# Kernel optimization log

Hardware: AMD Instinct MI355X
Metric: run time of the kernel (lower is better)

Reference implementation:

```python
import jax, jax.numpy as jnp
import numpy as np

N, D_IN, D_H, D_OUT, M = 256, 768, 768, 512, 100000


def setup_inputs() -> dict:
    key = jax.random.key(0)
    ks = jax.random.split(key, 8)
    img_feats = jax.random.normal(ks[0], (N, D_IN), dtype=jnp.float32)
    w1 = jax.random.normal(ks[1], (D_H, D_IN), dtype=jnp.float32) * (1.0 / np.sqrt(D_IN))
    b1 = jax.random.normal(ks[2], (D_H,), dtype=jnp.float32) * 0.01
    w2 = jax.random.normal(ks[3], (D_OUT, D_H), dtype=jnp.float32) * (1.0 / np.sqrt(D_H))
    b2 = jax.random.normal(ks[4], (D_OUT,), dtype=jnp.float32) * 0.01
    logit_scale = jnp.asarray(np.log(1.0 / 0.07), dtype=jnp.float32)
    loc = jax.random.normal(ks[5], (M, D_OUT), dtype=jnp.float32)
    loc_feats = loc / jnp.linalg.norm(loc, axis=1, keepdims=True)  # pre-normalized gallery
    gps_gallery = jax.random.uniform(ks[6], (M, 2), dtype=jnp.float32, minval=-90.0, maxval=90.0)
    return {
        "img_feats": img_feats, "w1": w1, "b1": b1, "w2": w2, "b2": b2,
        "logit_scale": logit_scale, "loc_feats": loc_feats,
        "gps_gallery": gps_gallery, "top_k": 5,
    }


def reference(img_feats, w1, b1, w2, b2, logit_scale, loc_feats, gps_gallery, top_k):
    # Tsfm MLP head: Linear -> ReLU -> Linear
    h = jax.nn.relu(img_feats @ w1.T + b1)            # [N, D_H]
    img = h @ w2.T + b2                               # [N, D_OUT]
    # F.normalize(dim=1)
    img_n = img / jnp.linalg.norm(img, axis=1, keepdims=True)
    # forward_cached: scaled cosine-similarity logits against 100K gallery
    logits = jnp.exp(logit_scale) * (img_n @ loc_feats.T)  # [N, M]
    # predict: softmax over full gallery row, then top-k retrieval
    probs = jax.nn.softmax(logits, axis=-1)
    top_vals, top_idx = jax.lax.top_k(probs, top_k)   # [N, k]
    top_pred_gps = gps_gallery[top_idx[0]]            # [k, 2] (first image, as in original)
    top_pred_prob = top_vals[0]                       # [k]
    return (logits, top_pred_gps, top_pred_prob)
```

## Files before the change

kernel.cpp:

```cpp
#include <hip/hip_runtime.h>
#include <math.h>

#define N_IMG 256
#define DIN   768
#define DH    768
#define DOUT  512
#define M_GAL 100000
#define CAP   2048
#define MT    784

typedef __bf16 bf16_t;
typedef __bf16 bf16x8 __attribute__((ext_vector_type(8)));
typedef float  f32x4  __attribute__((ext_vector_type(4)));

#define OFF_H      0
#define OFF_IMG    (N_IMG*DH)
#define OFF_IMGN   (OFF_IMG  + N_IMG*DOUT)
#define OFF_IMGT   (OFF_IMGN + N_IMG*DOUT)
#define OFF_STATS  (OFF_IMGT + N_IMG*DOUT/2)
#define OFF_CIDX   (OFF_STATS + 4)
#define OFF_CVAL   (OFF_CIDX + CAP)

#define OUT_GPS  ((size_t)N_IMG * (size_t)M_GAL)
#define OUT_PROB (OUT_GPS + 10)

__device__ inline unsigned fkey(float x) {
  unsigned u = __float_as_uint(x);
  return (u & 0x80000000u) ? ~u : (u | 0x80000000u);
}
__device__ inline float fkey_inv(unsigned k) {
  unsigned u = (k & 0x80000000u) ? (k ^ 0x80000000u) : ~k;
  return __uint_as_float(u);
}

template<int KDIM, int NCOLS, bool RELU>
__global__ __launch_bounds__(256) void mlp_gemm(const float* __restrict__ A,
    const float* __restrict__ B, const float* __restrict__ bias,
    float* __restrict__ C, unsigned* stats_init) {
  if (stats_init && blockIdx.x == 0 && blockIdx.y == 0 && threadIdx.x == 0) {
    stats_init[0] = 0u; stats_init[1] = 0u; stats_init[2] = 0u;
  }
  __shared__ float As[32][34];
  __shared__ float Bs[32][34];
  const int t  = threadIdx.x;
  const int rowbase = blockIdx.y * 32;
  const int colbase = blockIdx.x * 32;
  const int sm = t >> 3;
  const int kc = (t & 7) << 2;
  const int ty = t >> 4, tx = t & 15;
  float a00 = 0.f, a01 = 0.f, a10 = 0.f, a11 = 0.f;
  for (int kt = 0; kt < KDIM; kt += 32) {
    float4 av = *(const float4*)(A + (size_t)(rowbase + sm) * KDIM + kt + kc);
    float4 bv = *(const float4*)(B + (size_t)(colbase + sm) * KDIM + kt + kc);
    __syncthreads();
    As[kc+0][sm] = av.x; As[kc+1][sm] = av.y; As[kc+2][sm] = av.z; As[kc+3][sm] = av.w;
    Bs[kc+0][sm] = bv.x; Bs[kc+1][sm] = bv.y; Bs[kc+2][sm] = bv.z; Bs[kc+3][sm] = bv.w;
    __syncthreads();
#pragma unroll
    for (int j = 0; j < 32; ++j) {
      float2 a = *(const float2*)(&As[j][2*ty]);
      float2 b = *(const float2*)(&Bs[j][2*tx]);
      a00 = fmaf(a.x, b.x, a00); a01 = fmaf(a.x, b.y, a01);
      a10 = fmaf(a.y, b.x, a10); a11 = fmaf(a.y, b.y, a11);
    }
  }
  const int r0 = rowbase + 2*ty;
  const int c0 = colbase + 2*tx;
  const float bb0 = bias[c0], bb1 = bias[c0+1];
  float v00 = a00 + bb0, v01 = a01 + bb1, v10 = a10 + bb0, v11 = a11 + bb1;
  if (RELU) {
    v00 = fmaxf(v00, 0.f); v01 = fmaxf(v01, 0.f);
    v10 = fmaxf(v10, 0.f); v11 = fmaxf(v11, 0.f);
  }
  C[(size_t)r0*NCOLS + c0]       = v00; C[(size_t)r0*NCOLS + c0 + 1]     = v01;
  C[(size_t)(r0+1)*NCOLS + c0]   = v10; C[(size_t)(r0+1)*NCOLS + c0 + 1] = v11;
}

__global__ __launch_bounds__(256) void norm_cast_kernel(const float* __restrict__ img,
    float* __restrict__ img_n, bf16_t* __restrict__ img_t) {
  const int row = blockIdx.x, t = threadIdx.x;
  const float v0 = img[row*DOUT + t];
  const float v1 = img[row*DOUT + 256 + t];
  float s = v0*v0 + v1*v1;
  for (int o = 32; o > 0; o >>= 1) s += __shfl_down(s, o);
  __shared__ float ws4[4];
  if ((t & 63) == 0) ws4[t >> 6] = s;
  __syncthreads();
  const float tot = ws4[0] + ws4[1] + ws4[2] + ws4[3];
  const float inv = 1.0f / sqrtf(tot);
  const float n0 = v0 * inv, n1 = v1 * inv;
  img_n[row*DOUT + t]       = n0;
  img_n[row*DOUT + 256 + t] = n1;
  const int k0 = t, k1 = t + 256;
  img_t[(((k0 >> 3)*N_IMG) + row)*8 + (k0 & 7)] = (bf16_t)n0;
  img_t[(((k1 >> 3)*N_IMG) + row)*8 + (k1 & 7)] = (bf16_t)n1;
}

__global__ __launch_bounds__(256, 4) void logits_kernel(const float* __restrict__ loc,
    const bf16_t* __restrict__ img_t, const float* __restrict__ ls,
    float* __restrict__ out, float* __restrict__ sumexp, unsigned* __restrict__ maxkey) {
  __shared__ bf16_t Asl[32 * 64 * 8];
  const int t = threadIdx.x;
  const int w = t >> 6, l = t & 63;
  const int bx = blockIdx.x;
  const int mtile = (bx & 7) + (bx >> 5) * 8;
  const int ntile = (bx >> 3) & 3;
  const int mb = mtile * 128;
  const int nb = ntile * 64;
  const int lr = l & 15, lq = l >> 4;
  const int mw = mb + w * 32;

  const float* bp[2];
#pragma unroll
  for (int j = 0; j < 2; ++j) {
    int m = mw + j * 16 + lr;
    m = m < M_GAL ? m : (M_GAL - 1);
    bp[j] = loc + (size_t)m * 512 + lq * 8;
  }

  f32x4 acc[4][2];
#pragma unroll
  for (int i = 0; i < 4; ++i)
#pragma unroll
    for (int j = 0; j < 2; ++j)
      acc[i][j] = (f32x4){0.f, 0.f, 0.f, 0.f};

  float4 B0[3][2], B1[3][2];

#define ISSUE(kt) {                                                  \
    const int s_ = (kt) % 3;                                         \
    _Pragma("unroll")                                                \
    for (int j_ = 0; j_ < 2; ++j_) {                                 \
      const float* p_ = bp[j_] + (kt) * 32;                          \
      B0[s_][j_] = *(const float4*)p_;                               \
      B1[s_][j_] = *(const float4*)(p_ + 4);                         \
    } }

#define COMPUTE(kt) {                                                \
    const int kb_ = ((kt) & 7) * 4 + lq;                             \
    const int s_  = (kt) % 3;                                        \
    bf16x8 af_[4];                                                   \
    _Pragma("unroll")                                                \
    for (int i_ = 0; i_ < 4; ++i_)                                   \
      af_[i_] = *(const bf16x8*)(Asl + (kb_ * 64 + i_ * 16 + lr) * 8); \
    _Pragma("unroll")                                                \
    for (int j_ = 0; j_ < 2; ++j_) {                                 \
      bf16x8 bf_;                                                    \
      bf_[0] = (bf16_t)B0[s_][j_].x; bf_[1] = (bf16_t)B0[s_][j_].y;  \
      bf_[2] = (bf16_t)B0[s_][j_].z; bf_[3] = (bf16_t)B0[s_][j_].w;  \
      bf_[4] = (bf16_t)B1[s_][j_].x; bf_[5] = (bf16_t)B1[s_][j_].y;  \
      bf_[6] = (bf16_t)B1[s_][j_].z; bf_[7] = (bf16_t)B1[s_][j_].w;  \
      _Pragma("unroll")                                              \
      for (int i_ = 0; i_ < 4; ++i_)                                 \
        acc[i_][j_] = __builtin_amdgcn_mfma_f32_16x16x32_bf16(af_[i_], bf_, acc[i_][j_], 0, 0, 0); \
    } }

  ISSUE(0); ISSUE(1);
#pragma unroll
  for (int r = 0; r < 8; ++r) {
    const int c = r * 4 + w;
    __builtin_amdgcn_global_load_lds(
        (__attribute__((address_space(1))) void*)(img_t + ((size_t)c * N_IMG + nb + l) * 8),
        (__attribute__((address_space(3))) void*)(Asl + (c * 64 + l) * 8),
        16, 0, 0);
  }
  __syncthreads();

#pragma unroll
  for (int kt = 0; kt < 8; ++kt) {
    ISSUE(kt + 2);
    COMPUTE(kt);
  }

  __syncthreads();
#pragma unroll
  for (int r = 0; r < 8; ++r) {
    const int c = r * 4 + w;
    __builtin_amdgcn_global_load_lds(
        (__attribute__((address_space(1))) void*)(img_t + ((size_t)(32 + c) * N_IMG + nb + l) * 8),
        (__attribute__((address_space(3))) void*)(Asl + (c * 64 + l) * 8),
        16, 0, 0);
  }
  __syncthreads();

#pragma unroll
  for (int kt = 8; kt < 16; ++kt) {
    if (kt < 14) { ISSUE(kt + 2); }
    COMPUTE(kt);
  }
#undef ISSUE
#undef COMPUTE

  const float scale = expf(ls[0]);
  if (ntile == 0) {
    float mx = -1e30f, se = 0.f;
    if (lq == 0) {
#pragma unroll
      for (int j = 0; j < 2; ++j) {
        const int m = mw + j * 16 + lr;
        if (m < M_GAL) {
          const float v = scale * acc[0][j][0];
          mx = fmaxf(mx, v);
          se += expf(v);
        }
      }
    }
#pragma unroll
    for (int o = 1; o < 64; o <<= 1) {
      mx = fmaxf(mx, __shfl_xor(mx, o));
      se += __shfl_xor(se, o);
    }
    if (l == 0) { atomicAdd(sumexp, se); atomicMax(maxkey, fkey(mx)); }
  }
#pragma unroll
  for (int i = 0; i < 4; ++i) {
    const int imgr = nb + i * 16 + lq * 4;
#pragma unroll
    for (int j = 0; j < 2; ++j) {
      const int gal = mw + j * 16 + lr;
      if (gal < M_GAL) {
        const size_t base = (size_t)imgr * M_GAL + gal;
#pragma unroll
        for (int r = 0; r < 4; ++r)
          out[base + (size_t)r * M_GAL] = scale * acc[i][j][r];
      }
    }
  }
}

__global__ __launch_bounds__(256) void collect_kernel(const float* __restrict__ out,
    const unsigned* __restrict__ maxkey, unsigned* __restrict__ counter,
    int* __restrict__ cidx) {
  const int i = blockIdx.x * 256 + threadIdx.x;
  if (i >= M_GAL) return;
  const float thresh = fkey_inv(*maxkey) - 0.8f;
  if (out[i] > thresh) {
    const unsigned p = atomicAdd(counter, 1u);
    if (p < CAP) cidx[p] = i;
  }
}

__global__ __launch_bounds__(256) void recompute_kernel(const float* __restrict__ loc,
    const float* __restrict__ img_n, const float* __restrict__ ls,
    const unsigned* __restrict__ counter, const int* __restrict__ cidx,
    float* __restrict__ cval) {
  const int w = threadIdx.x >> 6, l = threadIdx.x & 63;
  const unsigned cnt = *counter;
  const int n = (int)(cnt < CAP ? cnt : CAP);
  const float scale = expf(ls[0]);
  for (int c = blockIdx.x * 4 + w; c < n; c += gridDim.x * 4) {
    const int idx = cidx[c];
    const float* B = loc + (size_t)idx * 512;
    float s = 0.f;
#pragma unroll
    for (int e = 0; e < 8; ++e) s = fmaf(img_n[l + e*64], B[l + e*64], s);
    for (int o = 32; o > 0; o >>= 1) s += __shfl_down(s, o);
    if (l == 0) cval[c] = scale * s;
  }
}

__global__ __launch_bounds__(256) void finalize_kernel(const unsigned* __restrict__ counter,
    const int* __restrict__ cidx, const float* __restrict__ cval,
    const float* __restrict__ gps, const float* __restrict__ sumexp,
    float* __restrict__ out) {
  __shared__ float v[CAP];
  __shared__ int   id[CAP];
  __shared__ float rv[256];
  __shared__ int   ri[256];
  __shared__ int   rs[256];
  const int t = threadIdx.x;
  const unsigned cnt = *counter;
  const int n = (int)(cnt < CAP ? cnt : CAP);
  for (int i = t; i < CAP; i += 256) {
    v[i]  = (i < n) ? cval[i] : -1e30f;
    id[i] = (i < n) ? cidx[i] : 0x7fffffff;
  }
  const float se = *sumexp;
  __syncthreads();
  for (int k = 0; k < 5; ++k) {
    float bv = -1e30f; int bidx = 0x7fffffff; int bslot = -1;
    for (int i = t; i < CAP; i += 256) {
      const float vi = v[i]; const int ii = id[i];
      if (vi > bv || (vi == bv && ii < bidx)) { bv = vi; bidx = ii; bslot = i; }
    }
    rv[t] = bv; ri[t] = bidx; rs[t] = bslot;
    __syncthreads();
    for (int s = 128; s > 0; s >>= 1) {
      if (t < s) {
        if (rv[t+s] > rv[t] || (rv[t+s] == rv[t] && ri[t+s] < ri[t])) {
          rv[t] = rv[t+s]; ri[t] = ri[t+s]; rs[t] = rs[t+s];
        }
      }
      __syncthreads();
    }
    if (t == 0) {
      const int sl = rs[0]; const int gi = ri[0]; const float lv = rv[0];
      float g0 = 0.f, g1 = 0.f, pr = 0.f;
      if (sl >= 0 && gi != 0x7fffffff) {
        g0 = gps[(size_t)gi*2]; g1 = gps[(size_t)gi*2 + 1];
        pr = expf(lv) / se;
        v[sl] = -1e30f; id[sl] = 0x7fffffff;
      }
      out[OUT_GPS + 2*k]     = g0;
      out[OUT_GPS + 2*k + 1] = g1;
      out[OUT_PROB + k]      = pr;
    }
    __syncthreads();
  }
}

extern "C" void kernel_launch(void* const* d_in, const int* in_sizes, int n_in,
                              void* d_out, int out_size, void* d_ws, size_t ws_size,
                              hipStream_t stream) {
  const float* img_feats = (const float*)d_in[0];
  const float* w1  = (const float*)d_in[1];
  const float* b1  = (const float*)d_in[2];
  const float* w2  = (const float*)d_in[3];
  const float* b2  = (const float*)d_in[4];
  const float* ls  = (const float*)d_in[5];
  const float* loc = (const float*)d_in[6];
  const float* gps = (const float*)d_in[7];
  float* out = (float*)d_out;
  float* ws  = (float*)d_ws;

  float*    h       = ws + OFF_H;
  float*    img     = ws + OFF_IMG;
  float*    img_n   = ws + OFF_IMGN;
  bf16_t*   img_t   = (bf16_t*)(ws + OFF_IMGT);
  float*    sumexp  = ws + OFF_STATS;
  unsigned* maxkey  = (unsigned*)(ws + OFF_STATS + 1);
  unsigned* counter = (unsigned*)(ws + OFF_STATS + 2);
  int*      cidx    = (int*)(ws + OFF_CIDX);
  float*    cval    = ws + OFF_CVAL;

  mlp_gemm<DIN, DH, true><<<dim3(DH/32, N_IMG/32), 256, 0, stream>>>(
      img_feats, w1, b1, h, (unsigned*)(ws + OFF_STATS));
  mlp_gemm<DH, DOUT, false><<<dim3(DOUT/32, N_IMG/32), 256, 0, stream>>>(
      h, w2, b2, img, nullptr);
  norm_cast_kernel<<<N_IMG, 256, 0, stream>>>(img, img_n, img_t);
  logits_kernel<<<MT * 4, 256, 0, stream>>>(loc, img_t, ls, out, sumexp, maxkey);
  collect_kernel<<<(M_GAL + 255) / 256, 256, 0, stream>>>(out, maxkey, counter, cidx);
  recompute_kernel<<<128, 256, 0, stream>>>(loc, img_n, ls, counter, cidx, cval);
  finalize_kernel<<<1, 256, 0, stream>>>(counter, cidx, cval, gps, sumexp, out);
}
```

Baseline: 474.8 us.

## Restructure logits GEMM to 64-gallery tiles covering all 256 images with 32x32 MFMA

The logits kernel now gives each block 64 gallery rows against all 256 image rows instead of 128 gallery rows against 64 images. Each gallery row is read from global memory once rather than by four separate n-tile blocks. It switches from 16x16x32 to 32x32x16 bf16 MFMA, and streams the image operand through LDS in eight k-chunks, with a pair of barriers between chunks. This cuts redundant fp32 gallery traffic and conversions, but adds more barriers and a larger accumulator per thread (64 floats), which may limit occupancy.

```diff
diff --git a/kernel.cpp b/kernel.cpp
--- a/kernel.cpp
+++ b/kernel.cpp
@@ -7,11 +7,12 @@
 #define DOUT  512
 #define M_GAL 100000
 #define CAP   2048
-#define MT    784
+#define MT    1568
 
 typedef __bf16 bf16_t;
 typedef __bf16 bf16x8 __attribute__((ext_vector_type(8)));
 typedef float  f32x4  __attribute__((ext_vector_type(4)));
+typedef float  f32x16 __attribute__((ext_vector_type(16)));
 
 #define OFF_H      0
 #define OFF_IMG    (N_IMG*DH)
@@ -99,111 +100,86 @@
 __global__ __launch_bounds__(256, 4) void logits_kernel(const float* __restrict__ loc,
     const bf16_t* __restrict__ img_t, const float* __restrict__ ls,
     float* __restrict__ out, float* __restrict__ sumexp, unsigned* __restrict__ maxkey) {
-  __shared__ bf16_t Asl[32 * 64 * 8];
+  __shared__ bf16_t Asl[8 * 256 * 8];
   const int t = threadIdx.x;
   const int w = t >> 6, l = t & 63;
-  const int bx = blockIdx.x;
-  const int mtile = (bx & 7) + (bx >> 5) * 8;
-  const int ntile = (bx >> 3) & 3;
-  const int mb = mtile * 128;
-  const int nb = ntile * 64;
-  const int lr = l & 15, lq = l >> 4;
-  const int mw = mb + w * 32;
-
-  const float* bp[2];
-#pragma unroll
-  for (int j = 0; j < 2; ++j) {
-    int m = mw + j * 16 + lr;
-    m = m < M_GAL ? m : (M_GAL - 1);
-    bp[j] = loc + (size_t)m * 512 + lq * 8;
-  }
-
-  f32x4 acc[4][2];
-#pragma unroll
-  for (int i = 0; i < 4; ++i)
-#pragma unroll
-    for (int j = 0; j < 2; ++j)
-      acc[i][j] = (f32x4){0.f, 0.f, 0.f, 0.f};
-
-  float4 B0[3][2], B1[3][2];
-
-#define ISSUE(kt) {                                                  \
-    const int s_ = (kt) % 3;                                         \
-    _Pragma("unroll")                                                \
-    for (int j_ = 0; j_ < 2; ++j_) {                                 \
-      const float* p_ = bp[j_] + (kt) * 32;                          \
-      B0[s_][j_] = *(const float4*)p_;                               \
-      B1[s_][j_] = *(const float4*)(p_ + 4);                         \
+  const int wr = w >> 1;
+  const int wc = w & 1;
+  const int hi = l >> 5;
+  const int lo = l & 31;
+  const int mb = blockIdx.x * 64;
+  const int m  = mb + wc * 32 + lo;
+  const int mc = m < M_GAL ? m : (M_GAL - 1);
+  const float* bp = loc + (size_t)mc * 512 + hi * 8;
+
+  f32x16 acc[4];
+#pragma unroll
+  for (int i = 0; i < 4; ++i) acc[i] = (f32x16)(0.f);
+
+  float4 B0[3], B1[3];
+
+#define ISSUE(kt) {                                                   \
+    const int s_ = (kt) % 3;                                          \
+    const float* p_ = bp + (kt) * 16;                                 \
+    B0[s_] = *(const float4*)p_;                                      \
+    B1[s_] = *(const float4*)(p_ + 4);                                \
+  }
+
+#define COMPUTE(kt) {                                                 \
+    const int s_  = (kt) % 3;                                         \
+    const int kl_ = ((kt) & 3) * 2 + hi;         \
+    bf16x8 af_[4];                                                    \
+    _Pragma("unroll")                                                 \
+    for (int i_ = 0; i_ < 4; ++i_)                                    \
+      af_[i_] = *(const bf16x8*)(Asl + (kl_ * 256 + wr * 128 + i_ * 32 + lo) * 8); \
+    bf16x8 bf_;                                                       \
+    bf_[0] = (bf16_t)B0[s_].x; bf_[1] = (bf16_t)B0[s_].y;             \
+    bf_[2] = (bf16_t)B0[s_].z; bf_[3] = (bf16_t)B0[s_].w;             \
+    bf_[4] = (bf16_t)B1[s_].x; bf_[5] = (bf16_t)B1[s_].y;             \
+    bf_[6] = (bf16_t)B1[s_].z; bf_[7] = (bf16_t)B1[s_].w;             \
+    _Pragma("unroll")                                                 \
+    for (int i_ = 0; i_ < 4; ++i_)                                    \
+      acc[i_] = __builtin_amdgcn_mfma_f32_32x32x16_bf16(af_[i_], bf_, acc[i_], 0, 0, 0); \
+  }
+
+#define STAGE(c_) {                                                   \
+    _Pragma("unroll")                                                 \
+    for (int r_ = 0; r_ < 8; ++r_) {                                  \
+      __builtin_amdgcn_global_load_lds(                               \
+          (__attribute__((address_space(1))) void*)(img_t + (((c_) * 8 + r_) * 256 + t) * 8), \
+          (__attribute__((address_space(3))) void*)(Asl + (r_ * 256 + t) * 8), \
+          16, 0, 0);                                                  \
     } }
 
-#define COMPUTE(kt) {                                                \
-    const int kb_ = ((kt) & 7) * 4 + lq;                             \
-    const int s_  = (kt) % 3;                                        \
-    bf16x8 af_[4];                                                   \
-    _Pragma("unroll")                                                \
-    for (int i_ = 0; i_ < 4; ++i_)                                   \
-      af_[i_] = *(const bf16x8*)(Asl + (kb_ * 64 + i_ * 16 + lr) * 8); \
-    _Pragma("unroll")                                                \
-    for (int j_ = 0; j_ < 2; ++j_) {                                 \
-      bf16x8 bf_;                                                    \
-      bf_[0] = (bf16_t)B0[s_][j_].x; bf_[1] = (bf16_t)B0[s_][j_].y;  \
-      bf_[2] = (bf16_t)B0[s_][j_].z; bf_[3] = (bf16_t)B0[s_][j_].w;  \
-      bf_[4] = (bf16_t)B1[s_][j_].x; bf_[5] = (bf16_t)B1[s_][j_].y;  \
-      bf_[6] = (bf16_t)B1[s_][j_].z; bf_[7] = (bf16_t)B1[s_][j_].w;  \
-      _Pragma("unroll")                                              \
-      for (int i_ = 0; i_ < 4; ++i_)                                 \
-        acc[i_][j_] = __builtin_amdgcn_mfma_f32_16x16x32_bf16(af_[i_], bf_, acc[i_][j_], 0, 0, 0); \
-    } }
-
   ISSUE(0); ISSUE(1);
-#pragma unroll
-  for (int r = 0; r < 8; ++r) {
-    const int c = r * 4 + w;
-    __builtin_amdgcn_global_load_lds(
-        (__attribute__((address_space(1))) void*)(img_t + ((size_t)c * N_IMG + nb + l) * 8),
-        (__attribute__((address_space(3))) void*)(Asl + (c * 64 + l) * 8),
-        16, 0, 0);
-  }
+  STAGE(0);
   __syncthreads();
 
 #pragma unroll
-  for (int kt = 0; kt < 8; ++kt) {
-    ISSUE(kt + 2);
-    COMPUTE(kt);
-  }
-
-  __syncthreads();
-#pragma unroll
-  for (int r = 0; r < 8; ++r) {
-    const int c = r * 4 + w;
-    __builtin_amdgcn_global_load_lds(
-        (__attribute__((address_space(1))) void*)(img_t + ((size_t)(32 + c) * N_IMG + nb + l) * 8),
-        (__attribute__((address_space(3))) void*)(Asl + (c * 64 + l) * 8),
-        16, 0, 0);
-  }
-  __syncthreads();
-
-#pragma unroll
-  for (int kt = 8; kt < 16; ++kt) {
-    if (kt < 14) { ISSUE(kt + 2); }
-    COMPUTE(kt);
+  for (int c = 0; c < 8; ++c) {
+#pragma unroll
+    for (int q = 0; q < 4; ++q) {
+      const int kt = c * 4 + q;
+      if (kt + 2 < 32) { ISSUE(kt + 2); }
+      COMPUTE(kt);
+    }
+    if (c < 7) {
+      __syncthreads();
+      STAGE(c + 1);
+      __syncthreads();
+    }
   }
 #undef ISSUE
 #undef COMPUTE
+#undef STAGE
 
   const float scale = expf(ls[0]);
-  if (ntile == 0) {
+  if (wr == 0) {
     float mx = -1e30f, se = 0.f;
-    if (lq == 0) {
-#pragma unroll
-      for (int j = 0; j < 2; ++j) {
-        const int m = mw + j * 16 + lr;
-        if (m < M_GAL) {
-          const float v = scale * acc[0][j][0];
-          mx = fmaxf(mx, v);
-          se += expf(v);
-        }
-      }
+    if (hi == 0 && m < M_GAL) {
+      const float v = scale * acc[0][0];
+      mx = v;
+      se = expf(v);
     }
 #pragma unroll
     for (int o = 1; o < 64; o <<= 1) {
@@ -212,17 +188,14 @@
     }
     if (l == 0) { atomicAdd(sumexp, se); atomicMax(maxkey, fkey(mx)); }
   }
-#pragma unroll
-  for (int i = 0; i < 4; ++i) {
-    const int imgr = nb + i * 16 + lq * 4;
-#pragma unroll
-    for (int j = 0; j < 2; ++j) {
-      const int gal = mw + j * 16 + lr;
-      if (gal < M_GAL) {
-        const size_t base = (size_t)imgr * M_GAL + gal;
-#pragma unroll
-        for (int r = 0; r < 4; ++r)
-          out[base + (size_t)r * M_GAL] = scale * acc[i][j][r];
+  if (m < M_GAL) {
+#pragma unroll
+    for (int i = 0; i < 4; ++i) {
+      const int ib = wr * 128 + i * 32 + hi * 4;
+#pragma unroll
+      for (int r = 0; r < 16; ++r) {
+        const int img = ib + (r & 3) + 8 * (r >> 2);
+        out[(size_t)img * M_GAL + m] = scale * acc[i][r];
       }
     }
   }
@@ -338,7 +311,7 @@
   mlp_gemm<DH, DOUT, false><<<dim3(DOUT/32, N_IMG/32), 256, 0, stream>>>(
       h, w2, b2, img, nullptr);
   norm_cast_kernel<<<N_IMG, 256, 0, stream>>>(img, img_n, img_t);
-  logits_kernel<<<MT * 4, 256, 0, stream>>>(loc, img_t, ls, out, sumexp, maxkey);
+  logits_kernel<<<MT, 256, 0, stream>>>(loc, img_t, ls, out, sumexp, maxkey);
   collect_kernel<<<(M_GAL + 255) / 256, 256, 0, stream>>>(out, maxkey, counter, cidx);
   recompute_kernel<<<128, 256, 0, stream>>>(loc, img_n, ls, counter, cidx, cval);
   finalize_kernel<<<1, 256, 0, stream>>>(counter, cidx, cval, gps, sumexp, out);
```

After: 452.7 us. 1.05x faster.
